# Performance work log

Hardware: AMD Instinct MI355X
Metric: run time of the kernel (lower is better)

The kernel has to match this reference:

```python
import jax, jax.numpy as jnp
import numpy as np

IC, HC, L, T, BS = 512, 512, 2, 512, 64
FORGET_BIAS = 1.0


def setup_inputs() -> dict:
    key = jax.random.key(0)
    k_x, k0, k1 = jax.random.split(key, 3)
    # xavier_normal std = sqrt(2/(fan_in+fan_out)), bias zeros (per module init)
    std0 = float(np.sqrt(2.0 / ((IC + HC) + 4 * HC)))
    std1 = float(np.sqrt(2.0 / ((HC + HC) + 4 * HC)))
    return {
        "x": jax.random.normal(k_x, (T, BS, IC), dtype=jnp.float32),
        "W0": jax.random.normal(k0, (IC + HC, 4 * HC), dtype=jnp.float32) * std0,
        "b0": jnp.zeros((4 * HC,), dtype=jnp.float32),
        "W1": jax.random.normal(k1, (HC + HC, 4 * HC), dtype=jnp.float32) * std1,
        "b1": jnp.zeros((4 * HC,), dtype=jnp.float32),
        "h0": jnp.zeros((L, 1, HC), dtype=jnp.float32),
        "c0": jnp.zeros((L, 1, HC), dtype=jnp.float32),
    }


def _run_layer(W, b, x_seq, h_init, c_init):
    def step(carry, xt):
        h, c = carry
        z = jnp.concatenate([xt, h], axis=1) @ W + b  # [bs, 4*hc]
        f, i, o, g = jnp.split(z, 4, axis=1)
        f = jax.nn.sigmoid(f + FORGET_BIAS)
        i = jax.nn.sigmoid(i)
        o = jax.nn.sigmoid(o)
        g = jnp.tanh(g)
        c = c * f + g * i
        h = o * jnp.tanh(c)
        return (h, c), h

    (hT, cT), hs = jax.lax.scan(step, (h_init, c_init), x_seq)
    return hs, hT, cT


def reference(x, W0, b0, W1, b1, h0, c0):
    bs = x.shape[1]
    h = jnp.broadcast_to(h0, (L, bs, HC))
    c = jnp.broadcast_to(c0, (L, bs, HC))
    params = [(W0, b0), (W1, b1)]
    lstm_input = x
    hs_final, cs_final = [], []
    for layer in range(L):
        W, b = params[layer]
        lstm_input, hT, cT = _run_layer(W, b, lstm_input, h[layer], c[layer])
        hs_final.append(hT)
        cs_final.append(cT)
    out = lstm_input  # [T, bs, hc]
    hs = jnp.stack(hs_final, axis=0)  # [L, bs, hc]
    cs = jnp.stack(cs_final, axis=0)
    return (out, (hs, cs))
```

## Files before the change

kernel.cpp:

```cpp
#include <hip/hip_runtime.h>
#include <cstdint>
#include <cstddef>


#define T_STEPS 512
#define WROW 1032

typedef float f32x4 __attribute__((ext_vector_type(4)));
typedef short s16x8 __attribute__((ext_vector_type(8)));

__device__ __forceinline__ unsigned short f2bf(float f) {
    unsigned int u = __builtin_bit_cast(unsigned int, f);
    u += 0x7FFFu + ((u >> 16) & 1u);
    return (unsigned short)(u >> 16);
}
__device__ __forceinline__ float sig_(float x)  { return 1.0f / (1.0f + __expf(-x)); }
__device__ __forceinline__ float tanh_(float x) { return 1.0f - 2.0f / (__expf(2.0f * x) + 1.0f); }

__device__ __forceinline__ s16x8 ldc(const unsigned short* p) {
    unsigned long long lo = __hip_atomic_load((unsigned long long*)p,     __ATOMIC_RELAXED, __HIP_MEMORY_SCOPE_AGENT);
    unsigned long long hi = __hip_atomic_load((unsigned long long*)p + 1, __ATOMIC_RELAXED, __HIP_MEMORY_SCOPE_AGENT);
    ulonglong2 u; u.x = lo; u.y = hi;
    return __builtin_bit_cast(s16x8, u);
}
__device__ __forceinline__ void stc(unsigned short* p, s16x8 v) {
    ulonglong2 u = __builtin_bit_cast(ulonglong2, v);
    __hip_atomic_store((unsigned long long*)p,     u.x, __ATOMIC_RELAXED, __HIP_MEMORY_SCOPE_AGENT);
    __hip_atomic_store((unsigned long long*)p + 1, u.y, __ATOMIC_RELAXED, __HIP_MEMORY_SCOPE_AGENT);
}
__device__ __forceinline__ void spin_eq(const unsigned int* p, unsigned int tag) {
    while (__hip_atomic_load(p, __ATOMIC_RELAXED, __HIP_MEMORY_SCOPE_AGENT) != tag)
        __builtin_amdgcn_s_sleep(1);
}


__global__ void k_conv_bf16(const float* __restrict__ src, unsigned short* __restrict__ dst) {
    int i = (blockIdx.x * 256 + threadIdx.x) * 8;
    float4 a = *(const float4*)(src + i);
    float4 b = *(const float4*)(src + i + 4);
    s16x8 o;
    o[0]=(short)f2bf(a.x); o[1]=(short)f2bf(a.y); o[2]=(short)f2bf(a.z); o[3]=(short)f2bf(a.w);
    o[4]=(short)f2bf(b.x); o[5]=(short)f2bf(b.y); o[6]=(short)f2bf(b.z); o[7]=(short)f2bf(b.w);
    *(s16x8*)(dst + i) = o;
}

__global__ void k_transpose_w(const float* __restrict__ W0, const float* __restrict__ W1,
                              unsigned short* __restrict__ WT0, unsigned short* __restrict__ WT1) {
    __shared__ unsigned short tile[32][33];
    const float* W = blockIdx.z ? W1 : W0;
    unsigned short* WT = blockIdx.z ? WT1 : WT0;
    int n0 = blockIdx.x * 32, k0 = blockIdx.y * 32;
    int tx = threadIdx.x, ty = threadIdx.y;
    #pragma unroll
    for (int i = 0; i < 4; i++)
        tile[ty + i*8][tx] = f2bf(W[(size_t)(k0 + ty + i*8) * 2048 + n0 + tx]);
    __syncthreads();
    #pragma unroll
    for (int i = 0; i < 4; i++)
        WT[(size_t)(n0 + ty + i*8) * 1024 + k0 + tx] = tile[tx][ty + i*8];
}

__global__ void k_hinit(const float* __restrict__ h0, unsigned short* __restrict__ hi0,
                        unsigned short* __restrict__ hi1) {
    int idx = blockIdx.x * 256 + threadIdx.x;
    int layer = idx >> 15;
    int r = idx & 32767;
    int b = r >> 9;
    int j = r & 511;
    unsigned short v = f2bf(h0[layer * 512 + j]);
    unsigned short* d = layer ? hi1 : hi0;
    d[(size_t)((j >> 3) * 64 + b) * 8 + (j & 7)] = v;
}

__global__ __launch_bounds__(256, 1) void k_lstm_fused(
    const unsigned short* __restrict__ xb,
    const unsigned short* __restrict__ hi0, const unsigned short* __restrict__ hi1,
    const unsigned short* __restrict__ WT0, const unsigned short* __restrict__ WT1,
    const float* __restrict__ b0, const float* __restrict__ b1,
    const float* __restrict__ c0,
    unsigned short* __restrict__ h0s, unsigned short* __restrict__ h1s,
    float* __restrict__ out, float* __restrict__ hs, float* __restrict__ cs,
    unsigned int* __restrict__ flags)
{
    __shared__ unsigned short Wl[32][WROW];
    __shared__ unsigned short hstage[64][8];

    const int isl1 = (int)(blockIdx.x >> 6);
    const int wg   = (int)(blockIdx.x & 63);
    const int tid  = threadIdx.x;
    const int j0   = wg * 8;

    const unsigned short* WT    = isl1 ? WT1 : WT0;
    const float*          bias  = isl1 ? b1  : b0;
    const float*          c0l   = c0 + isl1 * 512;
    const unsigned short* hinit = isl1 ? hi1 : hi0;
    unsigned short*       hseq  = isl1 ? h1s : h0s;
    unsigned int* fl_own  = flags + (size_t)isl1 * 512 * 64 * 16;
    unsigned int* fl_prod = flags;

    #pragma unroll
    for (int it = 0; it < 16; it++) {
        int idx = it * 256 + tid;
        int row = idx >> 7;
        int ch  = idx & 127;
        int cc_ = row & 15;
        int gate = (row >> 4) * 2 + (cc_ >> 3);
        int gr = gate * 512 + j0 + (cc_ & 7);
        *(s16x8*)(&Wl[row][ch * 8]) = *(const s16x8*)(WT + (size_t)gr * 1024 + ch * 8);
    }
    __syncthreads();

    const int lane = tid & 63;
    const int wv = tid >> 6;
    const int q = lane >> 4;
    const int cc = lane & 15;
    const int arow = wv * 16 + cc;
    const int jj = j0 + (cc & 7);
    const int bb = wv * 16 + q * 4;

    const float bias0 = (cc < 8) ? bias[jj] : bias[512 + jj];
    const float bias1 = (cc < 8) ? bias[1024 + jj] : bias[1536 + jj];
    float cst[4];
    {
        float ci = c0l[jj];
        cst[0] = cst[1] = cst[2] = cst[3] = ci;
    }

    for (int t = 0; t < T_STEPS; t++) {
        f32x4 acc0  = {bias0, bias0, bias0, bias0};
        f32x4 acc1  = {bias1, bias1, bias1, bias1};
        f32x4 acc0b = {0.f, 0.f, 0.f, 0.f};
        f32x4 acc1b = {0.f, 0.f, 0.f, 0.f};

        if (!isl1) {
            const unsigned short* xp = xb + (size_t)(t * 64 + arow) * 512 + q * 8;
            s16x8 ax[16];
            #pragma unroll
            for (int kk = 0; kk < 16; kk++)
                ax[kk] = *(const s16x8*)(xp + kk * 32);
            #pragma unroll
            for (int kk = 0; kk < 16; kk += 2) {
                s16x8 w00 = *(const s16x8*)(&Wl[cc][kk * 32 + q * 8]);
                s16x8 w10 = *(const s16x8*)(&Wl[16 + cc][kk * 32 + q * 8]);
                acc0  = __builtin_amdgcn_mfma_f32_16x16x32_bf16(ax[kk], w00, acc0, 0, 0, 0);
                acc1  = __builtin_amdgcn_mfma_f32_16x16x32_bf16(ax[kk], w10, acc1, 0, 0, 0);
                s16x8 w01 = *(const s16x8*)(&Wl[cc][(kk + 1) * 32 + q * 8]);
                s16x8 w11 = *(const s16x8*)(&Wl[16 + cc][(kk + 1) * 32 + q * 8]);
                acc0b = __builtin_amdgcn_mfma_f32_16x16x32_bf16(ax[kk + 1], w01, acc0b, 0, 0, 0);
                acc1b = __builtin_amdgcn_mfma_f32_16x16x32_bf16(ax[kk + 1], w11, acc1b, 0, 0, 0);
            }
            if (t > 0)
                spin_eq(fl_own + (size_t)(t - 1) * 64 * 16 + lane * 16, (unsigned int)t);
            const unsigned short* hb = t ? (hseq + (size_t)(t - 1) * 32768) : hinit;
            s16x8 ah[16];
            #pragma unroll
            for (int kk = 0; kk < 16; kk++)
                ah[kk] = ldc(hb + ((size_t)(kk * 4 + q) * 64 + arow) * 8);
            #pragma unroll
            for (int kk = 0; kk < 16; kk += 2) {
                s16x8 w00 = *(const s16x8*)(&Wl[cc][(16 + kk) * 32 + q * 8]);
                s16x8 w10 = *(const s16x8*)(&Wl[16 + cc][(16 + kk) * 32 + q * 8]);
                acc0  = __builtin_amdgcn_mfma_f32_16x16x32_bf16(ah[kk], w00, acc0, 0, 0, 0);
                acc1  = __builtin_amdgcn_mfma_f32_16x16x32_bf16(ah[kk], w10, acc1, 0, 0, 0);
                s16x8 w01 = *(const s16x8*)(&Wl[cc][(17 + kk) * 32 + q * 8]);
                s16x8 w11 = *(const s16x8*)(&Wl[16 + cc][(17 + kk) * 32 + q * 8]);
                acc0b = __builtin_amdgcn_mfma_f32_16x16x32_bf16(ah[kk + 1], w01, acc0b, 0, 0, 0);
                acc1b = __builtin_amdgcn_mfma_f32_16x16x32_bf16(ah[kk + 1], w11, acc1b, 0, 0, 0);
            }
        } else {
            if (t > 0)
                spin_eq(fl_own + (size_t)(t - 1) * 64 * 16 + lane * 16, (unsigned int)t);
            const unsigned short* hb = t ? (hseq + (size_t)(t - 1) * 32768) : hinit;
            s16x8 ah[16];
            #pragma unroll
            for (int kk = 0; kk < 16; kk++)
                ah[kk] = ldc(hb + ((size_t)(kk * 4 + q) * 64 + arow) * 8);
            #pragma unroll
            for (int kk = 0; kk < 16; kk += 2) {
                s16x8 w00 = *(const s16x8*)(&Wl[cc][(16 + kk) * 32 + q * 8]);
                s16x8 w10 = *(const s16x8*)(&Wl[16 + cc][(16 + kk) * 32 + q * 8]);
                acc0  = __builtin_amdgcn_mfma_f32_16x16x32_bf16(ah[kk], w00, acc0, 0, 0, 0);
                acc1  = __builtin_amdgcn_mfma_f32_16x16x32_bf16(ah[kk], w10, acc1, 0, 0, 0);
                s16x8 w01 = *(const s16x8*)(&Wl[cc][(17 + kk) * 32 + q * 8]);
                s16x8 w11 = *(const s16x8*)(&Wl[16 + cc][(17 + kk) * 32 + q * 8]);
                acc0b = __builtin_amdgcn_mfma_f32_16x16x32_bf16(ah[kk + 1], w01, acc0b, 0, 0, 0);
                acc1b = __builtin_amdgcn_mfma_f32_16x16x32_bf16(ah[kk + 1], w11, acc1b, 0, 0, 0);
            }
            spin_eq(fl_prod + (size_t)t * 64 * 16 + lane * 16, (unsigned int)(t + 1));
            const unsigned short* xp = h0s + (size_t)t * 32768;
            s16x8 ax[16];
            #pragma unroll
            for (int kk = 0; kk < 16; kk++)
                ax[kk] = ldc(xp + ((size_t)(kk * 4 + q) * 64 + arow) * 8);
            #pragma unroll
            for (int kk = 0; kk < 16; kk += 2) {
                s16x8 w00 = *(const s16x8*)(&Wl[cc][kk * 32 + q * 8]);
                s16x8 w10 = *(const s16x8*)(&Wl[16 + cc][kk * 32 + q * 8]);
                acc0  = __builtin_amdgcn_mfma_f32_16x16x32_bf16(ax[kk], w00, acc0, 0, 0, 0);
                acc1  = __builtin_amdgcn_mfma_f32_16x16x32_bf16(ax[kk], w10, acc1, 0, 0, 0);
                s16x8 w01 = *(const s16x8*)(&Wl[cc][(kk + 1) * 32 + q * 8]);
                s16x8 w11 = *(const s16x8*)(&Wl[16 + cc][(kk + 1) * 32 + q * 8]);
                acc0b = __builtin_amdgcn_mfma_f32_16x16x32_bf16(ax[kk + 1], w01, acc0b, 0, 0, 0);
                acc1b = __builtin_amdgcn_mfma_f32_16x16x32_bf16(ax[kk + 1], w11, acc1b, 0, 0, 0);
            }
        }
        acc0 = acc0 + acc0b;
        acc1 = acc1 + acc1b;

        float hv4[4];
        #pragma unroll
        for (int r = 0; r < 4; r++) {
            float z0 = acc0[r], z1 = acc1[r];
            float p0 = __shfl_xor(z0, 8, 64);
            float p1 = __shfl_xor(z1, 8, 64);
            float zf = (cc < 8) ? z0 : p0;
            float zi = (cc < 8) ? p0 : z0;
            float zo = (cc < 8) ? z1 : p1;
            float zg = (cc < 8) ? p1 : z1;
            float fg = sig_(zf + 1.0f);
            float ig = sig_(zi);
            float og = sig_(zo);
            float gg = tanh_(zg);
            float cn = cst[r] * fg + gg * ig;
            cst[r] = cn;
            float hv = og * tanh_(cn);
            hv4[r] = hv;
            if (cc < 8)
                hstage[bb + r][cc] = f2bf(hv);
        }

        {
            unsigned short* hdst = hseq + (size_t)t * 32768 + (size_t)wg * 512;
            if (lane < 16) {
                int row = wv * 16 + lane;
                s16x8 v = *(const s16x8*)(&hstage[row][0]);
                stc(hdst + (size_t)row * 8, v);
            }
        }
        __syncthreads();
        if (tid == 0)
            __hip_atomic_store(fl_own + (size_t)t * 64 * 16 + wg * 16,
                               (unsigned int)(t + 1), __ATOMIC_RELAXED, __HIP_MEMORY_SCOPE_AGENT);

        #pragma unroll
        for (int r = 0; r < 4; r++) {
            int b = bb + r;
            if (isl1 && cc >= 8)
                out[(size_t)(t * 64 + b) * 512 + jj] = hv4[r];
            if (t == T_STEPS - 1) {
                if (cc < 8) hs[(size_t)(isl1 * 64 + b) * 512 + jj] = hv4[r];
                else        cs[(size_t)(isl1 * 64 + b) * 512 + jj] = cst[r];
            }
        }
    }
}


extern "C" void kernel_launch(void* const* d_in, const int* in_sizes, int n_in,
                              void* d_out, int out_size, void* d_ws, size_t ws_size,
                              hipStream_t stream) {
    const float* x  = (const float*)d_in[0];
    const float* W0 = (const float*)d_in[1];
    const float* b0 = (const float*)d_in[2];
    const float* W1 = (const float*)d_in[3];
    const float* b1 = (const float*)d_in[4];
    const float* h0 = (const float*)d_in[5];
    const float* c0 = (const float*)d_in[6];
    float* out = (float*)d_out;

    char* ws = (char*)d_ws;
    unsigned short* xb  = (unsigned short*)(ws);
    unsigned short* h0s = (unsigned short*)(ws + 33554432);
    unsigned short* h1s = (unsigned short*)(ws + 2 * 33554432);
    unsigned short* WT0 = (unsigned short*)(ws + 3 * 33554432);
    unsigned short* WT1 = (unsigned short*)(ws + 3 * 33554432 + 4194304);
    unsigned short* hi0 = (unsigned short*)(ws + 3 * 33554432 + 2 * 4194304);
    unsigned short* hi1 = (unsigned short*)(ws + 3 * 33554432 + 2 * 4194304 + 65536);
    unsigned int*   flags = (unsigned int*)(ws + 3 * 33554432 + 2 * 4194304 + 2 * 65536);

    k_conv_bf16<<<8192, 256, 0, stream>>>(x, xb);
    k_transpose_w<<<dim3(64, 32, 2), dim3(32, 8), 0, stream>>>(W0, W1, WT0, WT1);
    k_hinit<<<256, 256, 0, stream>>>(h0, hi0, hi1);

    float* hs = out + 16777216;
    float* cs = hs + 65536;
    k_lstm_fused<<<128, 256, 0, stream>>>(xb, hi0, hi1, WT0, WT1, b0, b1, c0,
                                          h0s, h1s, out, hs, cs, flags);
}
```

Baseline: 2.906 ms.

## Pack step flags densely and replace atomic h loads with dependent plain loads

The per-block flags move from one flag per 64-byte line to a dense array, so each wave's 64 lanes poll 256 contiguous bytes instead of 64 separate cache lines. The hidden-state reads switch from pairs of 64-bit relaxed atomic loads to plain 128-bit vector loads. A fake data dependency (flag value XOR tag, always zero) is added to the address so the loads cannot be issued before the spin finishes. The spin sleep also grows from 1 to 2. The risk is correctness: relaxed flags with no acquire fence, plus plain loads that may be served from stale non-coherent caches.

After: 3.053 ms. 5.1% more time.

```diff
diff --git a/kernel.cpp b/kernel.cpp
--- a/kernel.cpp
+++ b/kernel.cpp
@@ -17,20 +17,18 @@
 __device__ __forceinline__ float sig_(float x)  { return 1.0f / (1.0f + __expf(-x)); }
 __device__ __forceinline__ float tanh_(float x) { return 1.0f - 2.0f / (__expf(2.0f * x) + 1.0f); }
 
-__device__ __forceinline__ s16x8 ldc(const unsigned short* p) {
-    unsigned long long lo = __hip_atomic_load((unsigned long long*)p,     __ATOMIC_RELAXED, __HIP_MEMORY_SCOPE_AGENT);
-    unsigned long long hi = __hip_atomic_load((unsigned long long*)p + 1, __ATOMIC_RELAXED, __HIP_MEMORY_SCOPE_AGENT);
-    ulonglong2 u; u.x = lo; u.y = hi;
-    return __builtin_bit_cast(s16x8, u);
-}
 __device__ __forceinline__ void stc(unsigned short* p, s16x8 v) {
     ulonglong2 u = __builtin_bit_cast(ulonglong2, v);
     __hip_atomic_store((unsigned long long*)p,     u.x, __ATOMIC_RELAXED, __HIP_MEMORY_SCOPE_AGENT);
     __hip_atomic_store((unsigned long long*)p + 1, u.y, __ATOMIC_RELAXED, __HIP_MEMORY_SCOPE_AGENT);
 }
-__device__ __forceinline__ void spin_eq(const unsigned int* p, unsigned int tag) {
-    while (__hip_atomic_load(p, __ATOMIC_RELAXED, __HIP_MEMORY_SCOPE_AGENT) != tag)
-        __builtin_amdgcn_s_sleep(1);
+__device__ __forceinline__ unsigned int spin_eq(const unsigned int* p, unsigned int tag) {
+    unsigned int v = __hip_atomic_load(p, __ATOMIC_RELAXED, __HIP_MEMORY_SCOPE_AGENT);
+    while (v != tag) {
+        __builtin_amdgcn_s_sleep(2);
+        v = __hip_atomic_load(p, __ATOMIC_RELAXED, __HIP_MEMORY_SCOPE_AGENT);
+    }
+    return v ^ tag;
 }
 
 
@@ -95,7 +93,7 @@
     const float*          c0l   = c0 + isl1 * 512;
     const unsigned short* hinit = isl1 ? hi1 : hi0;
     unsigned short*       hseq  = isl1 ? h1s : h0s;
-    unsigned int* fl_own  = flags + (size_t)isl1 * 512 * 64 * 16;
+    unsigned int* fl_own  = flags + (size_t)isl1 * 512 * 64;
     unsigned int* fl_prod = flags;
 
     #pragma unroll
@@ -149,13 +147,14 @@
                 acc0b = __builtin_amdgcn_mfma_f32_16x16x32_bf16(ax[kk + 1], w01, acc0b, 0, 0, 0);
                 acc1b = __builtin_amdgcn_mfma_f32_16x16x32_bf16(ax[kk + 1], w11, acc1b, 0, 0, 0);
             }
+            unsigned int dep = 0;
             if (t > 0)
-                spin_eq(fl_own + (size_t)(t - 1) * 64 * 16 + lane * 16, (unsigned int)t);
-            const unsigned short* hb = t ? (hseq + (size_t)(t - 1) * 32768) : hinit;
+                dep = spin_eq(fl_own + (size_t)(t - 1) * 64 + lane, (unsigned int)t);
+            const unsigned short* hb = (t ? (hseq + (size_t)(t - 1) * 32768) : hinit) + dep;
             s16x8 ah[16];
             #pragma unroll
             for (int kk = 0; kk < 16; kk++)
-                ah[kk] = ldc(hb + ((size_t)(kk * 4 + q) * 64 + arow) * 8);
+                ah[kk] = *(const s16x8*)(hb + ((size_t)(kk * 4 + q) * 64 + arow) * 8);
             #pragma unroll
             for (int kk = 0; kk < 16; kk += 2) {
                 s16x8 w00 = *(const s16x8*)(&Wl[cc][(16 + kk) * 32 + q * 8]);
@@ -168,13 +167,14 @@
                 acc1b = __builtin_amdgcn_mfma_f32_16x16x32_bf16(ah[kk + 1], w11, acc1b, 0, 0, 0);
             }
         } else {
+            unsigned int dep = 0;
             if (t > 0)
-                spin_eq(fl_own + (size_t)(t - 1) * 64 * 16 + lane * 16, (unsigned int)t);
-            const unsigned short* hb = t ? (hseq + (size_t)(t - 1) * 32768) : hinit;
+                dep = spin_eq(fl_own + (size_t)(t - 1) * 64 + lane, (unsigned int)t);
+            const unsigned short* hb = (t ? (hseq + (size_t)(t - 1) * 32768) : hinit) + dep;
             s16x8 ah[16];
             #pragma unroll
             for (int kk = 0; kk < 16; kk++)
-                ah[kk] = ldc(hb + ((size_t)(kk * 4 + q) * 64 + arow) * 8);
+                ah[kk] = *(const s16x8*)(hb + ((size_t)(kk * 4 + q) * 64 + arow) * 8);
             #pragma unroll
             for (int kk = 0; kk < 16; kk += 2) {
                 s16x8 w00 = *(const s16x8*)(&Wl[cc][(16 + kk) * 32 + q * 8]);
@@ -186,12 +186,12 @@
                 acc0b = __builtin_amdgcn_mfma_f32_16x16x32_bf16(ah[kk + 1], w01, acc0b, 0, 0, 0);
                 acc1b = __builtin_amdgcn_mfma_f32_16x16x32_bf16(ah[kk + 1], w11, acc1b, 0, 0, 0);
             }
-            spin_eq(fl_prod + (size_t)t * 64 * 16 + lane * 16, (unsigned int)(t + 1));
-            const unsigned short* xp = h0s + (size_t)t * 32768;
+            unsigned int dep2 = spin_eq(fl_prod + (size_t)t * 64 + lane, (unsigned int)(t + 1));
+            const unsigned short* xp = h0s + (size_t)t * 32768 + dep2;
             s16x8 ax[16];
             #pragma unroll
             for (int kk = 0; kk < 16; kk++)
-                ax[kk] = ldc(xp + ((size_t)(kk * 4 + q) * 64 + arow) * 8);
+                ax[kk] = *(const s16x8*)(xp + ((size_t)(kk * 4 + q) * 64 + arow) * 8);
             #pragma unroll
             for (int kk = 0; kk < 16; kk += 2) {
                 s16x8 w00 = *(const s16x8*)(&Wl[cc][kk * 32 + q * 8]);
@@ -239,7 +239,7 @@
         }
         __syncthreads();
         if (tid == 0)
-            __hip_atomic_store(fl_own + (size_t)t * 64 * 16 + wg * 16,
+            __hip_atomic_store(fl_own + (size_t)t * 64 + wg,
                                (unsigned int)(t + 1), __ATOMIC_RELAXED, __HIP_MEMORY_SCOPE_AGENT);
 
         #pragma unroll
```
